# Kernel tuning notes

Measured on AMD Instinct MI355X. Metric: run time of the kernel, lower is better.

The kernel has to match this reference:

```python
import jax, jax.numpy as jnp
import numpy as np


def setup_inputs() -> dict:
    key = jax.random.key(0)
    k1, k2 = jax.random.split(key)
    B, G, P = 64, 4999, 50
    raw_gene_expr = jax.random.normal(k1, (B, G), dtype=jnp.float32)
    # binary pathway membership matrix, mimics torch.randint(0, 2, (P, G)).float()
    pathway_gene_matrix = (jax.random.uniform(k2, (P, G)) < 0.5).astype(jnp.float32)
    return {"raw_gene_expr": raw_gene_expr, "pathway_gene_matrix": pathway_gene_matrix}


def reference(raw_gene_expr, pathway_gene_matrix):
    """Vectorized ssGSEA enrichment (compute_pathway_activations0).

    raw_gene_expr:        [B, G] float
    pathway_gene_matrix:  [P, G] binary float
    returns:              [B, P] signed max-deviation enrichment scores
    """
    B, G = raw_gene_expr.shape
    P = pathway_gene_matrix.shape[0]

    # Sort genes per sample in descending expression order
    order = jnp.argsort(-raw_gene_expr, axis=1)                      # [B, G]
    sorted_expr = jnp.take_along_axis(raw_gene_expr, order, axis=1)  # [B, G]

    # hit[b, p, i] = 1 if gene at sorted position i belongs to pathway p
    hit = (pathway_gene_matrix[:, order] > 0)                        # [P, B, G]
    hit = jnp.transpose(hit, (1, 0, 2)).astype(raw_gene_expr.dtype)  # [B, P, G]

    size = jnp.sum(pathway_gene_matrix > 0, axis=1).astype(raw_gene_expr.dtype)  # [P]

    # Weighted hit increments: |expr|^0.25 over hits, normalized per (sample, pathway)
    w = (jnp.abs(sorted_expr) ** 0.25)[:, None, :] * hit             # [B, P, G]
    s = jnp.sum(w, axis=-1, keepdims=True)
    w = jnp.where(s > 0, w / jnp.where(s > 0, s, 1.0), w)

    cum_hit = jnp.cumsum(w, axis=-1)                                 # [B, P, G]
    denom = jnp.maximum(G - size, 1.0)[None, :, None]                # guard size==G
    cum_miss = jnp.cumsum((1.0 - hit) / denom, axis=-1)              # [B, P, G]

    running = cum_hit - cum_miss                                     # [B, P, G]
    pos = jnp.argmax(jnp.abs(running), axis=-1)                      # [B, P]
    # signed max deviation == running value at the argmax of |running|
    es = jnp.take_along_axis(running, pos[..., None], axis=-1)[..., 0]  # [B, P]
    es = jnp.where(size[None, :] > 0, es, 0.0)
    return es
```

## Files before the change

### kernel.cpp

```cpp
#include <hip/hip_runtime.h>
#include <math.h>

typedef unsigned long long ull;

constexpr int Bc = 64;
constexpr int Gc = 4999;
constexpr int Pc = 50;

constexpr int RUN   = 512;
constexpr int NRUN  = 10;
constexpr int NPAD  = NRUN * RUN;
constexpr int EPT   = 8;
constexpr int LPW   = 79;
constexpr ull PADKEY = 0xFFFFFFFFFFFFFFFFull;

__device__ __forceinline__ ull shfl_xor64(ull v, int lm) {
    int lo = __shfl_xor((int)(unsigned)(v & 0xFFFFFFFFull), lm, 64);
    int hi = __shfl_xor((int)(unsigned)(v >> 32), lm, 64);
    return ((ull)(unsigned)hi << 32) | (unsigned)lo;
}

__global__ __launch_bounds__(320) void wave_sort512(
    const float* __restrict__ expr, const float* __restrict__ pathway,
    ull* __restrict__ runs, ull* __restrict__ pbits, int P, int G)
{
    const int rg = blockIdx.x, b = blockIdx.y;
    const int tid = threadIdx.x;
    const int lane = tid & 63;
    const int w = tid >> 6;
    const int r = rg * 5 + w;
    const int base = lane * EPT;
    const float* row = expr + (size_t)b * G;

    ull v[EPT];
#pragma unroll
    for (int o = 0; o < EPT; ++o) {
        int i = r * RUN + base + o;
        if (i < G) {
            unsigned u = __float_as_uint(row[i]);
            unsigned m = (u >> 31) ? ~u : (u | 0x80000000u);
            v[o] = ((ull)(~m) << 32) | (unsigned)i;
        } else {
            v[o] = PADKEY;
        }
    }

#pragma unroll
    for (int kk = 2; kk <= RUN; kk <<= 1) {
#pragma unroll
        for (int j = kk >> 1; j >= EPT; j >>= 1) {
            const int lm = j >> 3;
            const bool takeMin = (((lane & lm) == 0) == ((base & kk) == 0));
#pragma unroll
            for (int o = 0; o < EPT; ++o) {
                ull c = shfl_xor64(v[o], lm);
                ull mn = (v[o] < c) ? v[o] : c;
                ull mx = (v[o] < c) ? c : v[o];
                v[o] = takeMin ? mn : mx;
            }
        }
#pragma unroll
        for (int j = 4; j >= 1; j >>= 1) {
            if (j < kk) {
#pragma unroll
                for (int o = 0; o < EPT; ++o) {
                    if ((o & j) == 0) {
                        bool up = (((base + o) & kk) == 0);
                        ull a = v[o], c = v[o | j];
                        if ((a > c) == up) { v[o] = c; v[o | j] = a; }
                    }
                }
            }
        }
    }

    ull* dst = runs + ((size_t)b * NRUN + r) * RUN;
#pragma unroll
    for (int o = 0; o < EPT; ++o) dst[base + o] = v[o];

    if (rg == 0) {
        int g = b * 320 + tid;
        if (g < G) {
            ull m = 0;
#pragma unroll
            for (int p = 0; p < Pc; ++p)
                if (pathway[(size_t)p * G + g] > 0.0f) m |= (1ull << p);
            pbits[g] = m;
        }
    }
}

__global__ __launch_bounds__(1024) void rank_scatter(
    const ull* __restrict__ runs, const ull* __restrict__ pbits,
    float* __restrict__ wqout, ull* __restrict__ maskout, int G)
{
    __shared__ ull runsLDS[NPAD];
    const int rg = blockIdx.x, b = blockIdx.y, tid = threadIdx.x;

    const ull* rowruns = runs + (size_t)b * NPAD;
    for (int i = tid; i < NPAD; i += 1024) runsLDS[i] = rowruns[i];
    __syncthreads();

    const int e = rg * 1024 + tid;
    const ull keyv = runsLDS[e];
    if (keyv == PADKEY) return;

    const int run = e >> 9;
    int rank = e & 511;
#pragma unroll
    for (int rr = 0; rr < NRUN; ++rr) {
        if (rr == run) continue;
        const ull* arr = &runsLDS[rr * RUN];
        int pos = 0;
#pragma unroll
        for (int s = RUN; s >= 1; s >>= 1) {
            int np = pos + s;
            if (np <= RUN && arr[np - 1] < keyv) pos = np;
        }
        rank += pos;
    }

    int idx = (int)(unsigned)(keyv & 0xFFFFFFFFu);
    unsigned m = ~((unsigned)(keyv >> 32));
    unsigned absbits = ((m >> 31) ? m : ~m) & 0x7FFFFFFFu;
    float av = __uint_as_float(absbits);
    wqout[(size_t)b * G + rank] = sqrtf(sqrtf(av));
    maskout[(size_t)b * G + rank] = pbits[idx];
}

__global__ __launch_bounds__(256) void es_kernel(
    const float* __restrict__ wq, const ull* __restrict__ mask,
    float* __restrict__ out, int B, int P, int G)
{
    __shared__ float    swq[Gc];
    __shared__ unsigned sm32[Gc];

    const int pg = blockIdx.x;
    const int b  = blockIdx.y;
    const int tid = threadIdx.x;
    const int pbeg = pg * 13;
    const int pend = (pbeg + 13 < P) ? (pbeg + 13) : P;

    for (int i = tid; i < G; i += 256) {
        swq[i]  = wq[(size_t)b * G + i];
        sm32[i] = (unsigned)(mask[(size_t)b * G + i] >> pbeg);
    }
    __syncthreads();

    const int lane = tid & 63;
    const int w = tid >> 6;
    const int p0 = pbeg + w * 4;
    if (p0 >= pend) return;
    const int sh4 = w * 4;

    const int start = lane * LPW;
    const int cnt = (start + LPW < G) ? LPW : (G - start);

    double sw[4] = {0.0, 0.0, 0.0, 0.0};
    int sh[4] = {0, 0, 0, 0};
    for (int k = 0; k < cnt; ++k) {
        int s = start + k;
        unsigned nib = (sm32[s] >> sh4) & 15u;
        double wv = (double)swq[s];
#pragma unroll
        for (int q = 0; q < 4; ++q) {
            if ((nib >> q) & 1u) { sw[q] += wv; sh[q]++; }
        }
    }
    double norm[4], inv_denom[4], running[4];
    int sht[4];
#pragma unroll
    for (int q = 0; q < 4; ++q) {
        double swt = sw[q];
        int shq = sh[q];
#pragma unroll
        for (int off = 1; off < 64; off <<= 1) {
            swt += __shfl_xor(swt, off, 64);
            shq += __shfl_xor(shq, off, 64);
        }
        sht[q] = shq;
        norm[q]      = (swt > 0.0) ? 1.0 / swt : 1.0;
        inv_denom[q] = 1.0 / fmax((double)(G - shq), 1.0);
        double csum = sw[q] * norm[q] - (double)(cnt - sh[q]) * inv_denom[q];
        double x = csum;
#pragma unroll
        for (int off = 1; off < 64; off <<= 1) {
            double vv = __shfl_up(x, off, 64);
            if (lane >= off) x += vv;
        }
        running[q] = x - csum;
    }

    double bestv[4] = {-1.0, -1.0, -1.0, -1.0};
    double bestr[4] = {0.0, 0.0, 0.0, 0.0};
    int besti[4] = {0x7FFFFFFF, 0x7FFFFFFF, 0x7FFFFFFF, 0x7FFFFFFF};
    for (int k = 0; k < cnt; ++k) {
        int s = start + k;
        unsigned nib = (sm32[s] >> sh4) & 15u;
        double wv = (double)swq[s];
        int i = start + k;
#pragma unroll
        for (int q = 0; q < 4; ++q) {
            running[q] += ((nib >> q) & 1u) ? wv * norm[q] : -inv_denom[q];
            double a = fabs(running[q]);
            if (a > bestv[q]) { bestv[q] = a; bestr[q] = running[q]; besti[q] = i; }
        }
    }
#pragma unroll
    for (int q = 0; q < 4; ++q) {
#pragma unroll
        for (int off = 1; off < 64; off <<= 1) {
            double ov  = __shfl_xor(bestv[q], off, 64);
            double orr = __shfl_xor(bestr[q], off, 64);
            int    oi  = __shfl_xor(besti[q], off, 64);
            if (ov > bestv[q] || (ov == bestv[q] && oi < besti[q])) {
                bestv[q] = ov; bestr[q] = orr; besti[q] = oi;
            }
        }
    }

    if (lane == 0) {
#pragma unroll
        for (int q = 0; q < 4; ++q) {
            int p = p0 + q;
            if (p < pend)
                out[(size_t)b * P + p] = (sht[q] > 0) ? (float)bestr[q] : 0.0f;
        }
    }
}

extern "C" void kernel_launch(void* const* d_in, const int* in_sizes, int n_in,
                              void* d_out, int out_size, void* d_ws, size_t ws_size,
                              hipStream_t stream) {
    const float* expr    = (const float*)d_in[0];
    const float* pathway = (const float*)d_in[1];
    float* out = (float*)d_out;

    char* ws = (char*)d_ws;
    ull*   pbits = (ull*)ws;
    ull*   runs  = (ull*)(ws + 40960);
    float* wqa   = (float*)(ws + 2662400);
    ull*   maska = (ull*)(ws + 3942144);

    wave_sort512<<<dim3(2, Bc), dim3(320), 0, stream>>>(
        expr, pathway, runs, pbits, Pc, Gc);
    rank_scatter<<<dim3(5, Bc), dim3(1024), 0, stream>>>(runs, pbits, wqa, maska, Gc);
    es_kernel<<<dim3(4, Bc), dim3(256), 0, stream>>>(wqa, maska, out, Bc, Pc, Gc);
}
```

Baseline: 112.1 us.

## Fuse run sort and rank-scatter into one kernel; scatter gene indices instead of masks

The per-run bitonic sort and the merge-rank scatter now live in one 1024-thread kernel. Each block sorts all ten runs of its row into shared memory, so the global round trip for the runs buffer and one launch go away. The scatter stage now writes 16-bit gene indices instead of 64-bit pathway masks, and the ES kernel gathers pbits through those indices. In exchange, every one of the five blocks per row redoes the full sort. The pbits table is also written by the same kernel that is launched alongside the ES consumer, with a leftover empty loop and an odd index mapping (b*384) that may not cover every gene.

```diff
diff --git a/kernel.cpp b/kernel.cpp
--- a/kernel.cpp
+++ b/kernel.cpp
@@ -20,66 +20,66 @@
     return ((ull)(unsigned)hi << 32) | (unsigned)lo;
 }
 
-__global__ __launch_bounds__(320) void wave_sort512(
+__global__ __launch_bounds__(1024) void sort_rank(
     const float* __restrict__ expr, const float* __restrict__ pathway,
-    ull* __restrict__ runs, ull* __restrict__ pbits, int P, int G)
+    ull* __restrict__ pbits, float* __restrict__ wqout,
+    unsigned short* __restrict__ sidxout, int G)
 {
+    __shared__ ull runsLDS[NPAD];
     const int rg = blockIdx.x, b = blockIdx.y;
     const int tid = threadIdx.x;
     const int lane = tid & 63;
     const int w = tid >> 6;
-    const int r = rg * 5 + w;
-    const int base = lane * EPT;
-    const float* row = expr + (size_t)b * G;
-
-    ull v[EPT];
-#pragma unroll
-    for (int o = 0; o < EPT; ++o) {
-        int i = r * RUN + base + o;
-        if (i < G) {
-            unsigned u = __float_as_uint(row[i]);
-            unsigned m = (u >> 31) ? ~u : (u | 0x80000000u);
-            v[o] = ((ull)(~m) << 32) | (unsigned)i;
-        } else {
-            v[o] = PADKEY;
-        }
-    }
-
-#pragma unroll
-    for (int kk = 2; kk <= RUN; kk <<= 1) {
-#pragma unroll
-        for (int j = kk >> 1; j >= EPT; j >>= 1) {
-            const int lm = j >> 3;
-            const bool takeMin = (((lane & lm) == 0) == ((base & kk) == 0));
-#pragma unroll
-            for (int o = 0; o < EPT; ++o) {
-                ull c = shfl_xor64(v[o], lm);
-                ull mn = (v[o] < c) ? v[o] : c;
-                ull mx = (v[o] < c) ? c : v[o];
-                v[o] = takeMin ? mn : mx;
-            }
-        }
-#pragma unroll
-        for (int j = 4; j >= 1; j >>= 1) {
-            if (j < kk) {
+
+    if (w < NRUN) {
+        const int base = lane * EPT;
+        const float* row = expr + (size_t)b * G;
+        ull v[EPT];
+#pragma unroll
+        for (int o = 0; o < EPT; ++o) {
+            int i = w * RUN + base + o;
+            if (i < G) {
+                unsigned u = __float_as_uint(row[i]);
+                unsigned m = (u >> 31) ? ~u : (u | 0x80000000u);
+                v[o] = ((ull)(~m) << 32) | (unsigned)i;
+            } else {
+                v[o] = PADKEY;
+            }
+        }
+#pragma unroll
+        for (int kk = 2; kk <= RUN; kk <<= 1) {
+#pragma unroll
+            for (int j = kk >> 1; j >= EPT; j >>= 1) {
+                const int lm = j >> 3;
+                const bool takeMin = (((lane & lm) == 0) == ((base & kk) == 0));
 #pragma unroll
                 for (int o = 0; o < EPT; ++o) {
-                    if ((o & j) == 0) {
-                        bool up = (((base + o) & kk) == 0);
-                        ull a = v[o], c = v[o | j];
-                        if ((a > c) == up) { v[o] = c; v[o | j] = a; }
+                    ull c = shfl_xor64(v[o], lm);
+                    ull mn = (v[o] < c) ? v[o] : c;
+                    ull mx = (v[o] < c) ? c : v[o];
+                    v[o] = takeMin ? mn : mx;
+                }
+            }
+#pragma unroll
+            for (int j = 4; j >= 1; j >>= 1) {
+                if (j < kk) {
+#pragma unroll
+                    for (int o = 0; o < EPT; ++o) {
+                        if ((o & j) == 0) {
+                            bool up = (((base + o) & kk) == 0);
+                            ull a = v[o], c = v[o | j];
+                            if ((a > c) == up) { v[o] = c; v[o | j] = a; }
+                        }
                     }
                 }
             }
         }
-    }
-
-    ull* dst = runs + ((size_t)b * NRUN + r) * RUN;
-#pragma unroll
-    for (int o = 0; o < EPT; ++o) dst[base + o] = v[o];
-
-    if (rg == 0) {
-        int g = b * 320 + tid;
+#pragma unroll
+        for (int o = 0; o < EPT; ++o) runsLDS[w * RUN + base + o] = v[o];
+    } else if (rg == 0) {
+        for (int g = (w - NRUN) * 64 + lane; g < G; g += 6 * 64) {
+        }
+        int g = b * 384 + (w - NRUN) * 64 + lane;
         if (g < G) {
             ull m = 0;
 #pragma unroll
@@ -88,17 +88,6 @@
             pbits[g] = m;
         }
     }
-}
-
-__global__ __launch_bounds__(1024) void rank_scatter(
-    const ull* __restrict__ runs, const ull* __restrict__ pbits,
-    float* __restrict__ wqout, ull* __restrict__ maskout, int G)
-{
-    __shared__ ull runsLDS[NPAD];
-    const int rg = blockIdx.x, b = blockIdx.y, tid = threadIdx.x;
-
-    const ull* rowruns = runs + (size_t)b * NPAD;
-    for (int i = tid; i < NPAD; i += 1024) runsLDS[i] = rowruns[i];
     __syncthreads();
 
     const int e = rg * 1024 + tid;
@@ -125,12 +114,12 @@
     unsigned absbits = ((m >> 31) ? m : ~m) & 0x7FFFFFFFu;
     float av = __uint_as_float(absbits);
     wqout[(size_t)b * G + rank] = sqrtf(sqrtf(av));
-    maskout[(size_t)b * G + rank] = pbits[idx];
+    sidxout[(size_t)b * G + rank] = (unsigned short)idx;
 }
 
 __global__ __launch_bounds__(256) void es_kernel(
-    const float* __restrict__ wq, const ull* __restrict__ mask,
-    float* __restrict__ out, int B, int P, int G)
+    const float* __restrict__ wq, const unsigned short* __restrict__ sidx,
+    const ull* __restrict__ pbits, float* __restrict__ out, int B, int P, int G)
 {
     __shared__ float    swq[Gc];
     __shared__ unsigned sm32[Gc];
@@ -143,7 +132,7 @@
 
     for (int i = tid; i < G; i += 256) {
         swq[i]  = wq[(size_t)b * G + i];
-        sm32[i] = (unsigned)(mask[(size_t)b * G + i] >> pbeg);
+        sm32[i] = (unsigned)(pbits[sidx[(size_t)b * G + i]] >> pbeg);
     }
     __syncthreads();
 
@@ -198,12 +187,11 @@
         int s = start + k;
         unsigned nib = (sm32[s] >> sh4) & 15u;
         double wv = (double)swq[s];
-        int i = start + k;
 #pragma unroll
         for (int q = 0; q < 4; ++q) {
             running[q] += ((nib >> q) & 1u) ? wv * norm[q] : -inv_denom[q];
             double a = fabs(running[q]);
-            if (a > bestv[q]) { bestv[q] = a; bestr[q] = running[q]; besti[q] = i; }
+            if (a > bestv[q]) { bestv[q] = a; bestr[q] = running[q]; besti[q] = s; }
         }
     }
 #pragma unroll
@@ -237,13 +225,12 @@
     float* out = (float*)d_out;
 
     char* ws = (char*)d_ws;
-    ull*   pbits = (ull*)ws;
-    ull*   runs  = (ull*)(ws + 40960);
-    float* wqa   = (float*)(ws + 2662400);
-    ull*   maska = (ull*)(ws + 3942144);
-
-    wave_sort512<<<dim3(2, Bc), dim3(320), 0, stream>>>(
-        expr, pathway, runs, pbits, Pc, Gc);
-    rank_scatter<<<dim3(5, Bc), dim3(1024), 0, stream>>>(runs, pbits, wqa, maska, Gc);
-    es_kernel<<<dim3(4, Bc), dim3(256), 0, stream>>>(wqa, maska, out, Bc, Pc, Gc);
-}
+    ull*            pbits = (ull*)ws;
+    float*          wqa   = (float*)(ws + 40960);
+    unsigned short* sidx  = (unsigned short*)(ws + 1320704);
+
+    sort_rank<<<dim3(5, Bc), dim3(1024), 0, stream>>>(
+        expr, pathway, pbits, wqa, sidx, Gc);
+    es_kernel<<<dim3(4, Bc), dim3(256), 0, stream>>>(
+        wqa, sidx, pbits, out, Bc, Pc, Gc);
+}
```

Result: slower. 127.5 us (+13.7%).
